# Performance work log

Hardware: AMD Instinct MI355X
Metric: run time of the kernel (lower is better)

Reference implementation:

```python
import jax, jax.numpy as jnp
import numpy as np

CUTOFF = 3.0   # self.cutoff
RMIN = 3.5     # rmin in cutoff_function (note rmin > cutoff, faithful to source)
ETA = 4.0
N_RADIAL = 5
N_3BODY = 12
NATOMS = 2048
K = 48         # neighbors per atom (equal counts -> ragged loop becomes dense batch)
HID = 64
NPAIRS = NATOMS * K


def setup_inputs() -> dict:
    key = jax.random.key(0)
    ks = jax.random.split(key, 4)
    # displacements scaled so |rij| is mostly within a few Angstrom
    rij = jax.random.normal(ks[0], (NPAIRS, 3), jnp.float32) * 1.5
    # sorted-by-atom pair list with K neighbors per atom
    unique_i = jnp.repeat(jnp.arange(NATOMS, dtype=jnp.int64), K)
    W1 = jax.random.normal(ks[1], (N_RADIAL + N_3BODY, HID), jnp.float32) * 0.1
    b1 = jnp.zeros((HID,), jnp.float32)
    W2 = jax.random.normal(ks[2], (HID, HID), jnp.float32) * 0.1
    b2 = jnp.zeros((HID,), jnp.float32)
    W3 = jax.random.normal(ks[3], (HID, 1), jnp.float32) * 0.1
    b3 = jnp.zeros((1,), jnp.float32)
    return dict(rij=rij, unique_i=unique_i, W1=W1, b1=b1, W2=W2, b2=b2, W3=W3, b3=b3)


def _energy(rij, W1, b1, W2, b2, W3, b3):
    d = jnp.linalg.norm(rij, axis=1, keepdims=True)           # (P,1)
    diff_norm = rij / jnp.maximum(d, 1e-12)                   # F.normalize
    # pair cutoff (rmin=3.5, c=3.0 as in source)
    fc = jnp.where(d > RMIN,
                   0.5 + 0.5 * jnp.cos(jnp.pi * (d - RMIN) / (CUTOFF - RMIN)),
                   1.0)
    # radial Bessel basis, n = 1..5
    ns = jnp.arange(1, N_RADIAL + 1, dtype=rij.dtype)
    rbf = jnp.sqrt(2.0 / CUTOFF) * jnp.sin(ns * jnp.pi / CUTOFF * d) / d * fc  # (P,5)
    # 3-body Gaussian descriptors
    fcrik = (0.5 + 0.5 * jnp.cos(jnp.pi * d / CUTOFF))[:, 0]  # (P,)
    dn = diff_norm.reshape(NATOMS, K, 3)
    cosang = jnp.einsum('nkd,nld->nkl', dn, dn)               # (N,K,K) pairwise mm
    cosang = jnp.where(jnp.eye(K, dtype=bool)[None], 0.0, cosang)  # fill_diagonal_(0)
    mu = jnp.linspace(-1.0, 1.0, N_3BODY).astype(rij.dtype)
    w = fcrik.reshape(NATOMS, 1, K, 1)                        # fcrik broadcast on axis being summed
    g3b = jnp.sum(jnp.exp(-ETA * (cosang[..., None] - mu) ** 2) * w, axis=2)  # (N,K,12)
    g3b = g3b.reshape(NPAIRS, N_3BODY)
    desc = jnp.concatenate([rbf, g3b], axis=1)                # (P,17)
    h = jnp.tanh(desc @ W1 + b1)
    h = jnp.tanh(h @ W2 + b2)
    eij = h @ W3 + b3                                         # (P,1)
    return jnp.sum(eij * fc)


def reference(rij, unique_i, W1, b1, W2, b2, W3, b3):
    # Module output: gradients of total energy w.r.t. rij (written into beta)
    return jax.grad(_energy)(rij, W1, b1, W2, b2, W3, b3)
```

## Files before the change

### kernel.cpp

```cpp
#include <hip/hip_runtime.h>
#include <hip/hip_bf16.h>

#define NATOMS 2048
#define K 48
#define NR 5
#define NM 12
#define ND 17
#define HID 64

#define PI_F 3.14159265358979f
#define CUT 3.0f
#define RMIN_F 3.5f
#define AFC (-6.28318530717959f)
#define POC (PI_F / CUT)
#define SQ 0.816496580927726f
#define CMC (-0.132231404958678f)
#define N4L (-5.77078016355585f)
#define E1L (2.09846551402031f)
#define TL2 (2.88539008177793f)

__device__ unsigned short g_w1t[64 * 32];
__device__ unsigned short g_w2t[64 * 64];
__device__ unsigned short g_w2r[64 * 64];
__device__ unsigned short g_w1r[32 * 64];

using frag_ab = __attribute__((ext_vector_type(8))) short;
using frag_cd = __attribute__((ext_vector_type(4))) float;
using f2 = __attribute__((ext_vector_type(2))) float;
using f4 = __attribute__((ext_vector_type(4))) float;

__device__ __forceinline__ float fast_tanh(float x) {
    const float t = __builtin_amdgcn_exp2f(TL2 * x);
    return 1.0f - 2.0f * __builtin_amdgcn_rcpf(t + 1.0f);
}

__device__ __forceinline__ unsigned short f2bs(float x) {
    __hip_bfloat16 b = __float2bfloat16(x);
    return __builtin_bit_cast(unsigned short, b);
}

__device__ __forceinline__ float bs2f(unsigned short u) {
    return __builtin_bit_cast(float, ((unsigned)u) << 16);
}

template <int CTRL>
__device__ __forceinline__ float dpp_add(float x) {
    const int y = __builtin_amdgcn_update_dpp(
        0, __builtin_bit_cast(int, x), CTRL, 0xF, 0xF, true);
    return x + __builtin_bit_cast(float, y);
}

__global__ __launch_bounds__(256) void k_prep(const float* __restrict__ W1,
                                              const float* __restrict__ W2) {
    const int i = blockIdx.x * 256 + threadIdx.x;
    if (i < 2048) {
        const int n = i >> 5, k = i & 31;
        g_w1t[i] = (k < ND) ? f2bs(W1[k * HID + n]) : (unsigned short)0;
    } else if (i < 2048 + 4096) {
        const int j = i - 2048, n = j >> 6, k = j & 63;
        g_w2t[j] = f2bs(W2[k * HID + n]);
    } else if (i < 2048 + 8192) {
        const int j = i - (2048 + 4096);
        g_w2r[j] = f2bs(W2[j]);
    } else if (i < 2048 + 8192 + 2048) {
        const int j = i - (2048 + 8192), n = j >> 6;
        g_w1r[j] = (n < ND) ? f2bs(W1[j]) : (unsigned short)0;
    }
}

#define H1_OFF   0
#define ST_OFF   0
#define DESC_OFF 6912
#define GZ2_OFF  6912
#define SGD_OFF  6912
#define SGF_OFF  10560
#define SGU_OFF  11328
#define SS_OFF   13824
#define SE_OFF   18528
#define SU_OFF   19296
#define SFC_OFF  20064
#define SFK_OFF  20256
#define SM_BYTES 20448

__global__ __launch_bounds__(256, 6) void k_fused(const float* __restrict__ rij,
                                                  const float* __restrict__ b1,
                                                  const float* __restrict__ b2,
                                                  const float* __restrict__ W3,
                                                  const float* __restrict__ b3,
                                                  float* __restrict__ out) {
    __shared__ __align__(16) char smem[SM_BYTES];
    short*          h1S   = (short*)(smem + H1_OFF);
    unsigned short* sT    = (unsigned short*)(smem + ST_OFF);
    short*          descS = (short*)(smem + DESC_OFF);
    short*          gz2S  = (short*)(smem + GZ2_OFF);
    float*          sgd   = (float*)(smem + SGD_OFF);
    float*          sgf4  = (float*)(smem + SGF_OFF);
    float*          sgu4  = (float*)(smem + SGU_OFF);
    unsigned short* sS    = (unsigned short*)(smem + SS_OFF);
    float*          se    = (float*)(smem + SE_OFF);
    float*          su    = (float*)(smem + SU_OFF);
    float*          sfc   = (float*)(smem + SFC_OFF);
    float*          sfk   = (float*)(smem + SFK_OFF);

    const int t = threadIdx.x;
    const int base3 = blockIdx.x * (K * 3);
    const int w = t >> 6, lane = t & 63, quad = lane >> 4, lm = lane & 15;
    const int n0 = w * 16 + lm;

    const frag_ab wf1  = *(const frag_ab*)&g_w1t[n0 * 32 + quad * 8];
    const frag_ab wf2a = *(const frag_ab*)&g_w2t[n0 * 64 + quad * 8];
    const frag_ab wf2b = *(const frag_ab*)&g_w2t[n0 * 64 + 32 + quad * 8];
    const frag_ab wr2a = *(const frag_ab*)&g_w2r[n0 * 64 + quad * 8];
    const frag_ab wr2b = *(const frag_ab*)&g_w2r[n0 * 64 + 32 + quad * 8];
    const float bias1 = b1[n0];
    const float bias2 = b2[n0];
    const float w3n   = W3[n0];
    const float b3v   = b3[0];

    if (t < K) {
        const float x = rij[base3 + 3 * t];
        const float y = rij[base3 + 3 * t + 1];
        const float z = rij[base3 + 3 * t + 2];
        float s2 = fmaxf(x * x + y * y + z * z, 1e-24f);
        const float inv = __builtin_amdgcn_rsqf(s2);
        const float d = s2 * inv;
        *(f4*)&su[4 * t] = (f4){x * inv, y * inv, z * inv, d};
        sfk[t] = 0.5f + 0.5f * __cosf(POC * d);
        const float fc = (d > RMIN_F) ? (0.5f + 0.5f * __cosf(AFC * (d - RMIN_F))) : 1.0f;
        sfc[t] = fc;
        float s1, c1;
        __sincosf(POC * d, &s1, &c1);
        const float sc = SQ * fc * inv;
        float sn = s1, cn = c1;
#pragma unroll 1
        for (int n = 0; n < NR; n++) {
            descS[t * 40 + n] = (short)f2bs(sc * sn);
            const float snx = sn * c1 + cn * s1;
            cn = cn * c1 - sn * s1;
            sn = snx;
        }
#pragma unroll 1
        for (int c = ND; c < 32; c++) descS[t * 40 + c] = 0;
    }
    __syncthreads();

    if (t < 192) {
        const int k = t >> 2, ch = t & 3;
        const f4 uk = *(const f4*)&su[4 * k];
        const float* sul = &su[4 * (ch * 12)];
        f2 partv[6];
#pragma unroll
        for (int i = 0; i < 6; i++) partv[i] = (f2){0.0f, 0.0f};
#pragma unroll 1
        for (int li = 0; li < 12; li++) {
            const int l = ch * 12 + li;
            const f4 ul = *(const f4*)&sul[4 * li];
            float c = uk.x * ul.x + uk.y * ul.y + uk.z * ul.z;
            if (k == l) c = 0.0f;
            const float cp1 = c + 1.0f;
            const float e0 = __builtin_amdgcn_exp2f(N4L * cp1 * cp1) * sfk[l];
            const float e1 = __builtin_amdgcn_exp2f(E1L * cp1);
            const float e2s = e1 * e1;
            const f2 e2v = {e2s, e2s};
            f2 tm = {e0, e0 * e1};
            partv[0] += tm;
#pragma unroll
            for (int i = 1; i < 6; i++) { tm *= e2v; partv[i] += tm; }
        }
#pragma unroll
        for (int i = 0; i < 6; i++) {
            partv[i].x = dpp_add<0x4E>(dpp_add<0xB1>(partv[i].x));
            partv[i].y = dpp_add<0x4E>(dpp_add<0xB1>(partv[i].y));
        }
        if (ch == 0) {
#pragma unroll
            for (int i = 0; i < 6; i++) {
                const int m0 = 2 * i, m1 = 2 * i + 1;
                descS[k * 40 + NR + m0] =
                    (short)f2bs(partv[i].x * __expf(CMC * (float)(m0 * m0)));
                descS[k * 40 + NR + m1] =
                    (short)f2bs(partv[i].y * __expf(CMC * (float)(m1 * m1)));
            }
        }
    }
    __syncthreads();

#pragma unroll 1
    for (int mt = 0; mt < 3; mt++) {
        const frag_ab a = *(const frag_ab*)&descS[(mt * 16 + lm) * 40 + quad * 8];
        frag_cd acc = {bias1, bias1, bias1, bias1};
        acc = __builtin_amdgcn_mfma_f32_16x16x32_bf16(a, wf1, acc, 0, 0, 0);
#pragma unroll
        for (int r = 0; r < 4; r++)
            h1S[(mt * 16 + quad * 4 + r) * 72 + n0] = (short)f2bs(fast_tanh(acc[r]));
    }
    __syncthreads();

#pragma unroll 1
    for (int mt = 0; mt < 3; mt++) {
        const frag_ab a0 = *(const frag_ab*)&h1S[(mt * 16 + lm) * 72 + quad * 8];
        const frag_ab a1 = *(const frag_ab*)&h1S[(mt * 16 + lm) * 72 + 32 + quad * 8];
        frag_cd acc = {bias2, bias2, bias2, bias2};
        acc = __builtin_amdgcn_mfma_f32_16x16x32_bf16(a0, wf2a, acc, 0, 0, 0);
        acc = __builtin_amdgcn_mfma_f32_16x16x32_bf16(a1, wf2b, acc, 0, 0, 0);
        float ep[4];
#pragma unroll
        for (int r = 0; r < 4; r++) {
            const int row = mt * 16 + quad * 4 + r;
            const float tv = fast_tanh(acc[r]);
            ep[r] = tv * w3n;
            gz2S[row * 72 + n0] = (short)f2bs(sfc[row] * w3n * (1.0f - tv * tv));
        }
#pragma unroll
        for (int r = 0; r < 4; r++)
            ep[r] = dpp_add<0x118>(dpp_add<0x114>(dpp_add<0x112>(dpp_add<0x111>(ep[r]))));
        if (lm == 15) {
#pragma unroll
            for (int r = 0; r < 4; r++) se[w * 48 + mt * 16 + quad * 4 + r] = ep[r];
        }
    }
    __syncthreads();

#pragma unroll 1
    for (int mt = 0; mt < 3; mt++) {
        const frag_ab a0 = *(const frag_ab*)&gz2S[(mt * 16 + lm) * 72 + quad * 8];
        const frag_ab a1 = *(const frag_ab*)&gz2S[(mt * 16 + lm) * 72 + 32 + quad * 8];
        frag_cd acc = {0.0f, 0.0f, 0.0f, 0.0f};
        acc = __builtin_amdgcn_mfma_f32_16x16x32_bf16(a0, wr2a, acc, 0, 0, 0);
        acc = __builtin_amdgcn_mfma_f32_16x16x32_bf16(a1, wr2b, acc, 0, 0, 0);
#pragma unroll
        for (int r = 0; r < 4; r++) {
            const int row = mt * 16 + quad * 4 + r;
            const float tv = bs2f((unsigned short)h1S[row * 72 + n0]);
            h1S[row * 72 + n0] = (short)f2bs(acc[r] * (1.0f - tv * tv));
        }
    }
    __syncthreads();

#pragma unroll 1
    for (int tid = w; tid < 6; tid += 4) {
        const int mt = tid >> 1, nt = tid & 1, n = nt * 16 + lm;
        const frag_ab b0 = *(const frag_ab*)&g_w1r[n * 64 + quad * 8];
        const frag_ab b1f = *(const frag_ab*)&g_w1r[n * 64 + 32 + quad * 8];
        const frag_ab a0 = *(const frag_ab*)&h1S[(mt * 16 + lm) * 72 + quad * 8];
        const frag_ab a1 = *(const frag_ab*)&h1S[(mt * 16 + lm) * 72 + 32 + quad * 8];
        frag_cd acc = {0.0f, 0.0f, 0.0f, 0.0f};
        acc = __builtin_amdgcn_mfma_f32_16x16x32_bf16(a0, b0, acc, 0, 0, 0);
        acc = __builtin_amdgcn_mfma_f32_16x16x32_bf16(a1, b1f, acc, 0, 0, 0);
        if (n < ND) {
            const int mm = n - NR;
            const float cmul = (n >= NR) ? __expf(CMC * (float)(mm * mm)) : 1.0f;
#pragma unroll
            for (int r = 0; r < 4; r++)
                sgd[(mt * 16 + quad * 4 + r) * 19 + n] = acc[r] * cmul;
        }
    }
    if (t < K)
        sgd[t * 19 + 17] = se[t] + se[48 + t] + se[96 + t] + se[144 + t] + b3v;
    __syncthreads();

    if (t < 192) {
        const int k = t >> 2, ch = t & 3;
        f2 gm[NM];
#pragma unroll
        for (int m = 0; m < NM; m++) {
            const float g = sgd[k * 19 + NR + m];
            gm[m] = (f2){g, (float)m * g};
        }
        const f4 uk = *(const f4*)&su[4 * k];
        const float* sul = &su[4 * (ch * 12)];
#pragma unroll 1
        for (int li = 0; li < 12; li++) {
            const int l = ch * 12 + li;
            const f4 ul = *(const f4*)&sul[4 * li];
            float c = uk.x * ul.x + uk.y * ul.y + uk.z * ul.z;
            if (k == l) c = 0.0f;
            const float cp1 = c + 1.0f;
            const float e0 = __builtin_amdgcn_exp2f(N4L * cp1 * cp1);
            const float x = __builtin_amdgcn_exp2f(E1L * cp1);
            const f2 xx = {x, x};
            f2 pd = gm[11];
#pragma unroll
            for (int m = 10; m >= 1; m--) pd = __builtin_elementwise_fma(pd, xx, gm[m]);
            const float Pv = fmaf(pd.x, x, gm[0].x);
            const float T = e0 * Pv;
            const float U = e0 * x * pd.y;
            const float Sp = fmaf(cp1, T, -(2.0f / 11.0f) * U);
            const float Sv = (k == l) ? 0.0f : (-8.0f) * Sp;
            sT[k * 49 + l] = f2bs(T);
            sS[k * 49 + l] = f2bs(Sv);
        }
    }
    __syncthreads();

    if (lane < K) {
        float s = 0.0f;
#pragma unroll 1
        for (int kk = 12 * w; kk < 12 * w + 12; kk++) s += bs2f(sT[kk * 49 + lane]);
        sgf4[w * 48 + lane] = s;

        const int k = lane;
        const float fk = sfk[k];
        float gx = 0.0f, gy = 0.0f, gz = 0.0f;
#pragma unroll 1
        for (int l = 12 * w; l < 12 * w + 12; l++) {
            const float wgt = fmaf(bs2f(sS[k * 49 + l]), sfk[l],
                                   bs2f(sS[l * 49 + k]) * fk);
            const f4 ul = *(const f4*)&su[4 * l];
            gx = fmaf(wgt, ul.x, gx);
            gy = fmaf(wgt, ul.y, gy);
            gz = fmaf(wgt, ul.z, gz);
        }
        sgu4[(w * 48 + k) * 3 + 0] = gx;
        sgu4[(w * 48 + k) * 3 + 1] = gy;
        sgu4[(w * 48 + k) * 3 + 2] = gz;
    }
    __syncthreads();

    if (t < K) {
        const float sgf_t = sgf4[t] + sgf4[48 + t] + sgf4[96 + t] + sgf4[144 + t];
        float gux = 0.0f, guy = 0.0f, guz = 0.0f;
#pragma unroll
        for (int ww = 0; ww < 4; ww++) {
            gux += sgu4[(ww * 48 + t) * 3 + 0];
            guy += sgu4[(ww * 48 + t) * 3 + 1];
            guz += sgu4[(ww * 48 + t) * 3 + 2];
        }
        const f4 uv = *(const f4*)&su[4 * t];
        const float d = uv.w;
        const float ux = uv.x, uy = uv.y, uz = uv.z;
        const float invd = __builtin_amdgcn_rcpf(d);
        float gfc = sgd[t * 19 + 17];
        float gdR = 0.0f;
        float s1, c1;
        __sincosf(POC * d, &s1, &c1);
        float sn = s1, cn = c1, bn = POC;
#pragma unroll 1
        for (int n = 0; n < NR; n++) {
            const float g = sgd[t * 19 + n];
            gfc = fmaf(g, SQ * sn * invd, gfc);
            gdR = fmaf(g, SQ * (bn * cn - sn * invd) * invd, gdR);
            const float snx = sn * c1 + cn * s1;
            cn = cn * c1 - sn * s1;
            sn = snx;
            bn += POC;
        }
        const float fc = sfc[t];
        float dfc = 0.0f;
        if (d > RMIN_F) dfc = -0.5f * AFC * __sinf(AFC * (d - RMIN_F));
        const float dfcrik = -0.5f * POC * __sinf(POC * d);

        const float gd = fc * gdR + gfc * dfc + sgf_t * dfcrik;
        const float dot = gux * ux + guy * uy + guz * uz;

        out[base3 + 3 * t + 0] = fmaf(gd, ux, (gux - dot * ux) * invd);
        out[base3 + 3 * t + 1] = fmaf(gd, uy, (guy - dot * uy) * invd);
        out[base3 + 3 * t + 2] = fmaf(gd, uz, (guz - dot * uz) * invd);
    }
}

extern "C" void kernel_launch(void* const* d_in, const int* in_sizes, int n_in,
                              void* d_out, int out_size, void* d_ws, size_t ws_size,
                              hipStream_t stream) {
    (void)in_sizes; (void)n_in; (void)out_size; (void)d_ws; (void)ws_size;
    const float* rij = (const float*)d_in[0];
    const float* W1 = (const float*)d_in[2];
    const float* b1 = (const float*)d_in[3];
    const float* W2 = (const float*)d_in[4];
    const float* b2 = (const float*)d_in[5];
    const float* W3 = (const float*)d_in[6];
    const float* b3 = (const float*)d_in[7];
    float* out = (float*)d_out;

    k_prep<<<48, 256, 0, stream>>>(W1, W2);
    k_fused<<<NATOMS, 256, 0, stream>>>(rij, b1, b2, W3, b3, out);
}
```

Baseline: 93.49 us.

## Run each atom's block as a single wavefront without barriers

Shrinks each atom's block from four wavefronts to one 64-lane wavefront that does all MLP column tiles itself, which removes every __syncthreads and the cross-wave partial-sum buffers. The 3-body forward and backward loops now walk all 48 neighbors per lane instead of splitting across four lanes. Intermediate T/S matrices are stored transposed, so the symmetric gradient term is built from one direct accumulation plus a vectorized row read. The cost is less parallelism per atom, longer serial loops per lane and higher register pressure, traded against more resident blocks per CU.

```diff
diff --git a/kernel.cpp b/kernel.cpp
--- a/kernel.cpp
+++ b/kernel.cpp
@@ -28,6 +28,7 @@
 using frag_cd = __attribute__((ext_vector_type(4))) float;
 using f2 = __attribute__((ext_vector_type(2))) float;
 using f4 = __attribute__((ext_vector_type(4))) float;
+using s4 = __attribute__((ext_vector_type(4))) short;
 
 __device__ __forceinline__ float fast_tanh(float x) {
     const float t = __builtin_amdgcn_exp2f(TL2 * x);
@@ -69,92 +70,81 @@
 }
 
 #define H1_OFF   0
-#define ST_OFF   0
-#define DESC_OFF 6912
+#define TT_OFF   0
+#define SST_OFF  4992
 #define GZ2_OFF  6912
-#define SGD_OFF  6912
-#define SGF_OFF  10560
-#define SGU_OFF  11328
-#define SS_OFF   13824
-#define SE_OFF   18528
-#define SU_OFF   19296
-#define SFC_OFF  20064
-#define SFK_OFF  20256
-#define SM_BYTES 20448
-
-__global__ __launch_bounds__(256, 6) void k_fused(const float* __restrict__ rij,
-                                                  const float* __restrict__ b1,
-                                                  const float* __restrict__ b2,
-                                                  const float* __restrict__ W3,
-                                                  const float* __restrict__ b3,
-                                                  float* __restrict__ out) {
+#define DESC_OFF 13824
+#define SGD_OFF  13824
+#define SU_OFF   17664
+#define SFC_OFF  18432
+#define SFK_OFF  18624
+#define SM_BYTES 18816
+
+__global__ __launch_bounds__(64, 2) void k_fused(const float* __restrict__ rij,
+                                                 const float* __restrict__ b1,
+                                                 const float* __restrict__ b2,
+                                                 const float* __restrict__ W3,
+                                                 const float* __restrict__ b3,
+                                                 float* __restrict__ out) {
     __shared__ __align__(16) char smem[SM_BYTES];
     short*          h1S   = (short*)(smem + H1_OFF);
-    unsigned short* sT    = (unsigned short*)(smem + ST_OFF);
+    unsigned short* tT    = (unsigned short*)(smem + TT_OFF);
+    unsigned short* tS    = (unsigned short*)(smem + SST_OFF);
+    short*          gz2S  = (short*)(smem + GZ2_OFF);
     short*          descS = (short*)(smem + DESC_OFF);
-    short*          gz2S  = (short*)(smem + GZ2_OFF);
     float*          sgd   = (float*)(smem + SGD_OFF);
-    float*          sgf4  = (float*)(smem + SGF_OFF);
-    float*          sgu4  = (float*)(smem + SGU_OFF);
-    unsigned short* sS    = (unsigned short*)(smem + SS_OFF);
-    float*          se    = (float*)(smem + SE_OFF);
     float*          su    = (float*)(smem + SU_OFF);
     float*          sfc   = (float*)(smem + SFC_OFF);
     float*          sfk   = (float*)(smem + SFK_OFF);
 
-    const int t = threadIdx.x;
+    const int lane = threadIdx.x;
+    const int quad = lane >> 4, lm = lane & 15;
     const int base3 = blockIdx.x * (K * 3);
-    const int w = t >> 6, lane = t & 63, quad = lane >> 4, lm = lane & 15;
-    const int n0 = w * 16 + lm;
-
-    const frag_ab wf1  = *(const frag_ab*)&g_w1t[n0 * 32 + quad * 8];
-    const frag_ab wf2a = *(const frag_ab*)&g_w2t[n0 * 64 + quad * 8];
-    const frag_ab wf2b = *(const frag_ab*)&g_w2t[n0 * 64 + 32 + quad * 8];
-    const frag_ab wr2a = *(const frag_ab*)&g_w2r[n0 * 64 + quad * 8];
-    const frag_ab wr2b = *(const frag_ab*)&g_w2r[n0 * 64 + 32 + quad * 8];
-    const float bias1 = b1[n0];
-    const float bias2 = b2[n0];
-    const float w3n   = W3[n0];
-    const float b3v   = b3[0];
-
-    if (t < K) {
-        const float x = rij[base3 + 3 * t];
-        const float y = rij[base3 + 3 * t + 1];
-        const float z = rij[base3 + 3 * t + 2];
+
+    float b1v[4], b2v[4], w3v[4];
+#pragma unroll
+    for (int nt = 0; nt < 4; nt++) {
+        b1v[nt] = b1[nt * 16 + lm];
+        b2v[nt] = b2[nt * 16 + lm];
+        w3v[nt] = W3[nt * 16 + lm];
+    }
+    const float b3v = b3[0];
+
+    if (lane < K) {
+        const float x = rij[base3 + 3 * lane];
+        const float y = rij[base3 + 3 * lane + 1];
+        const float z = rij[base3 + 3 * lane + 2];
         float s2 = fmaxf(x * x + y * y + z * z, 1e-24f);
         const float inv = __builtin_amdgcn_rsqf(s2);
         const float d = s2 * inv;
-        *(f4*)&su[4 * t] = (f4){x * inv, y * inv, z * inv, d};
-        sfk[t] = 0.5f + 0.5f * __cosf(POC * d);
+        *(f4*)&su[4 * lane] = (f4){x * inv, y * inv, z * inv, d};
+        sfk[lane] = 0.5f + 0.5f * __cosf(POC * d);
         const float fc = (d > RMIN_F) ? (0.5f + 0.5f * __cosf(AFC * (d - RMIN_F))) : 1.0f;
-        sfc[t] = fc;
+        sfc[lane] = fc;
         float s1, c1;
         __sincosf(POC * d, &s1, &c1);
         const float sc = SQ * fc * inv;
         float sn = s1, cn = c1;
 #pragma unroll 1
         for (int n = 0; n < NR; n++) {
-            descS[t * 40 + n] = (short)f2bs(sc * sn);
+            descS[lane * 40 + n] = (short)f2bs(sc * sn);
             const float snx = sn * c1 + cn * s1;
             cn = cn * c1 - sn * s1;
             sn = snx;
         }
 #pragma unroll 1
-        for (int c = ND; c < 32; c++) descS[t * 40 + c] = 0;
-    }
-    __syncthreads();
-
-    if (t < 192) {
-        const int k = t >> 2, ch = t & 3;
+        for (int c = ND; c < 32; c++) descS[lane * 40 + c] = 0;
+    }
+
+    if (lane < K) {
+        const int k = lane;
         const f4 uk = *(const f4*)&su[4 * k];
-        const float* sul = &su[4 * (ch * 12)];
         f2 partv[6];
 #pragma unroll
         for (int i = 0; i < 6; i++) partv[i] = (f2){0.0f, 0.0f};
 #pragma unroll 1
-        for (int li = 0; li < 12; li++) {
-            const int l = ch * 12 + li;
-            const f4 ul = *(const f4*)&sul[4 * li];
+        for (int l = 0; l < K; l++) {
+            const f4 ul = *(const f4*)&su[4 * l];
             float c = uk.x * ul.x + uk.y * ul.y + uk.z * ul.z;
             if (k == l) c = 0.0f;
             const float cp1 = c + 1.0f;
@@ -169,110 +159,144 @@
         }
 #pragma unroll
         for (int i = 0; i < 6; i++) {
-            partv[i].x = dpp_add<0x4E>(dpp_add<0xB1>(partv[i].x));
-            partv[i].y = dpp_add<0x4E>(dpp_add<0xB1>(partv[i].y));
-        }
-        if (ch == 0) {
-#pragma unroll
-            for (int i = 0; i < 6; i++) {
-                const int m0 = 2 * i, m1 = 2 * i + 1;
-                descS[k * 40 + NR + m0] =
-                    (short)f2bs(partv[i].x * __expf(CMC * (float)(m0 * m0)));
-                descS[k * 40 + NR + m1] =
-                    (short)f2bs(partv[i].y * __expf(CMC * (float)(m1 * m1)));
-            }
-        }
-    }
-    __syncthreads();
-
-#pragma unroll 1
-    for (int mt = 0; mt < 3; mt++) {
-        const frag_ab a = *(const frag_ab*)&descS[(mt * 16 + lm) * 40 + quad * 8];
-        frag_cd acc = {bias1, bias1, bias1, bias1};
-        acc = __builtin_amdgcn_mfma_f32_16x16x32_bf16(a, wf1, acc, 0, 0, 0);
-#pragma unroll
-        for (int r = 0; r < 4; r++)
-            h1S[(mt * 16 + quad * 4 + r) * 72 + n0] = (short)f2bs(fast_tanh(acc[r]));
-    }
-    __syncthreads();
-
-#pragma unroll 1
-    for (int mt = 0; mt < 3; mt++) {
-        const frag_ab a0 = *(const frag_ab*)&h1S[(mt * 16 + lm) * 72 + quad * 8];
-        const frag_ab a1 = *(const frag_ab*)&h1S[(mt * 16 + lm) * 72 + 32 + quad * 8];
-        frag_cd acc = {bias2, bias2, bias2, bias2};
-        acc = __builtin_amdgcn_mfma_f32_16x16x32_bf16(a0, wf2a, acc, 0, 0, 0);
-        acc = __builtin_amdgcn_mfma_f32_16x16x32_bf16(a1, wf2b, acc, 0, 0, 0);
-        float ep[4];
-#pragma unroll
-        for (int r = 0; r < 4; r++) {
-            const int row = mt * 16 + quad * 4 + r;
-            const float tv = fast_tanh(acc[r]);
-            ep[r] = tv * w3n;
-            gz2S[row * 72 + n0] = (short)f2bs(sfc[row] * w3n * (1.0f - tv * tv));
-        }
-#pragma unroll
-        for (int r = 0; r < 4; r++)
-            ep[r] = dpp_add<0x118>(dpp_add<0x114>(dpp_add<0x112>(dpp_add<0x111>(ep[r]))));
-        if (lm == 15) {
-#pragma unroll
-            for (int r = 0; r < 4; r++) se[w * 48 + mt * 16 + quad * 4 + r] = ep[r];
-        }
-    }
-    __syncthreads();
-
-#pragma unroll 1
-    for (int mt = 0; mt < 3; mt++) {
-        const frag_ab a0 = *(const frag_ab*)&gz2S[(mt * 16 + lm) * 72 + quad * 8];
-        const frag_ab a1 = *(const frag_ab*)&gz2S[(mt * 16 + lm) * 72 + 32 + quad * 8];
-        frag_cd acc = {0.0f, 0.0f, 0.0f, 0.0f};
-        acc = __builtin_amdgcn_mfma_f32_16x16x32_bf16(a0, wr2a, acc, 0, 0, 0);
-        acc = __builtin_amdgcn_mfma_f32_16x16x32_bf16(a1, wr2b, acc, 0, 0, 0);
-#pragma unroll
-        for (int r = 0; r < 4; r++) {
-            const int row = mt * 16 + quad * 4 + r;
-            const float tv = bs2f((unsigned short)h1S[row * 72 + n0]);
-            h1S[row * 72 + n0] = (short)f2bs(acc[r] * (1.0f - tv * tv));
-        }
-    }
-    __syncthreads();
-
-#pragma unroll 1
-    for (int tid = w; tid < 6; tid += 4) {
-        const int mt = tid >> 1, nt = tid & 1, n = nt * 16 + lm;
-        const frag_ab b0 = *(const frag_ab*)&g_w1r[n * 64 + quad * 8];
-        const frag_ab b1f = *(const frag_ab*)&g_w1r[n * 64 + 32 + quad * 8];
-        const frag_ab a0 = *(const frag_ab*)&h1S[(mt * 16 + lm) * 72 + quad * 8];
-        const frag_ab a1 = *(const frag_ab*)&h1S[(mt * 16 + lm) * 72 + 32 + quad * 8];
-        frag_cd acc = {0.0f, 0.0f, 0.0f, 0.0f};
-        acc = __builtin_amdgcn_mfma_f32_16x16x32_bf16(a0, b0, acc, 0, 0, 0);
-        acc = __builtin_amdgcn_mfma_f32_16x16x32_bf16(a1, b1f, acc, 0, 0, 0);
-        if (n < ND) {
-            const int mm = n - NR;
-            const float cmul = (n >= NR) ? __expf(CMC * (float)(mm * mm)) : 1.0f;
+            const int m0 = 2 * i, m1 = 2 * i + 1;
+            descS[k * 40 + NR + m0] = (short)f2bs(partv[i].x * __expf(CMC * (float)(m0 * m0)));
+            descS[k * 40 + NR + m1] = (short)f2bs(partv[i].y * __expf(CMC * (float)(m1 * m1)));
+        }
+    }
+
+    {
+        frag_ab wf1[4];
+#pragma unroll
+        for (int nt = 0; nt < 4; nt++)
+            wf1[nt] = *(const frag_ab*)&g_w1t[(nt * 16 + lm) * 32 + quad * 8];
+#pragma unroll 1
+        for (int mt = 0; mt < 3; mt++) {
+            const frag_ab a = *(const frag_ab*)&descS[(mt * 16 + lm) * 40 + quad * 8];
+#pragma unroll
+            for (int nt = 0; nt < 4; nt++) {
+                frag_cd acc = {b1v[nt], b1v[nt], b1v[nt], b1v[nt]};
+                acc = __builtin_amdgcn_mfma_f32_16x16x32_bf16(a, wf1[nt], acc, 0, 0, 0);
+#pragma unroll
+                for (int r = 0; r < 4; r++)
+                    h1S[(mt * 16 + quad * 4 + r) * 72 + nt * 16 + lm] =
+                        (short)f2bs(fast_tanh(acc[r]));
+            }
+        }
+    }
+
+    {
+        frag_ab wa[4], wb[4];
+#pragma unroll
+        for (int nt = 0; nt < 4; nt++) {
+            wa[nt] = *(const frag_ab*)&g_w2t[(nt * 16 + lm) * 64 + quad * 8];
+            wb[nt] = *(const frag_ab*)&g_w2t[(nt * 16 + lm) * 64 + 32 + quad * 8];
+        }
+#pragma unroll 1
+        for (int mt = 0; mt < 3; mt++) {
+            const frag_ab a0 = *(const frag_ab*)&h1S[(mt * 16 + lm) * 72 + quad * 8];
+            const frag_ab a1 = *(const frag_ab*)&h1S[(mt * 16 + lm) * 72 + 32 + quad * 8];
+            const f4 fcv = *(const f4*)&sfc[mt * 16 + quad * 4];
+            float ep[4] = {0.0f, 0.0f, 0.0f, 0.0f};
+#pragma unroll
+            for (int nt = 0; nt < 4; nt++) {
+                frag_cd acc = {b2v[nt], b2v[nt], b2v[nt], b2v[nt]};
+                acc = __builtin_amdgcn_mfma_f32_16x16x32_bf16(a0, wa[nt], acc, 0, 0, 0);
+                acc = __builtin_amdgcn_mfma_f32_16x16x32_bf16(a1, wb[nt], acc, 0, 0, 0);
+#pragma unroll
+                for (int r = 0; r < 4; r++) {
+                    const int row = mt * 16 + quad * 4 + r;
+                    const float tv = fast_tanh(acc[r]);
+                    ep[r] = fmaf(tv, w3v[nt], ep[r]);
+                    gz2S[row * 72 + nt * 16 + lm] =
+                        (short)f2bs(fcv[r] * w3v[nt] * (1.0f - tv * tv));
+                }
+            }
 #pragma unroll
             for (int r = 0; r < 4; r++)
-                sgd[(mt * 16 + quad * 4 + r) * 19 + n] = acc[r] * cmul;
-        }
-    }
-    if (t < K)
-        sgd[t * 19 + 17] = se[t] + se[48 + t] + se[96 + t] + se[144 + t] + b3v;
-    __syncthreads();
-
-    if (t < 192) {
-        const int k = t >> 2, ch = t & 3;
+                ep[r] = dpp_add<0x118>(dpp_add<0x114>(dpp_add<0x112>(dpp_add<0x111>(ep[r]))));
+            if (lm == 15) {
+#pragma unroll
+                for (int r = 0; r < 4; r++)
+                    sgd[(mt * 16 + quad * 4 + r) * 20 + 17] = ep[r] + b3v;
+            }
+        }
+    }
+
+    {
+        frag_ab wa[4], wb[4];
+#pragma unroll
+        for (int nt = 0; nt < 4; nt++) {
+            wa[nt] = *(const frag_ab*)&g_w2r[(nt * 16 + lm) * 64 + quad * 8];
+            wb[nt] = *(const frag_ab*)&g_w2r[(nt * 16 + lm) * 64 + 32 + quad * 8];
+        }
+#pragma unroll 1
+        for (int mt = 0; mt < 3; mt++) {
+            const frag_ab a0 = *(const frag_ab*)&gz2S[(mt * 16 + lm) * 72 + quad * 8];
+            const frag_ab a1 = *(const frag_ab*)&gz2S[(mt * 16 + lm) * 72 + 32 + quad * 8];
+#pragma unroll
+            for (int nt = 0; nt < 4; nt++) {
+                frag_cd acc = {0.0f, 0.0f, 0.0f, 0.0f};
+                acc = __builtin_amdgcn_mfma_f32_16x16x32_bf16(a0, wa[nt], acc, 0, 0, 0);
+                acc = __builtin_amdgcn_mfma_f32_16x16x32_bf16(a1, wb[nt], acc, 0, 0, 0);
+#pragma unroll
+                for (int r = 0; r < 4; r++) {
+                    const int idx = (mt * 16 + quad * 4 + r) * 72 + nt * 16 + lm;
+                    const float tv = bs2f((unsigned short)h1S[idx]);
+                    h1S[idx] = (short)f2bs(acc[r] * (1.0f - tv * tv));
+                }
+            }
+        }
+    }
+
+    {
+        frag_ab wa[2], wb[2];
+#pragma unroll
+        for (int nt = 0; nt < 2; nt++) {
+            wa[nt] = *(const frag_ab*)&g_w1r[(nt * 16 + lm) * 64 + quad * 8];
+            wb[nt] = *(const frag_ab*)&g_w1r[(nt * 16 + lm) * 64 + 32 + quad * 8];
+        }
+        const float cm0 = (lm >= NR)
+            ? __expf(CMC * (float)((lm - NR) * (lm - NR))) : 1.0f;
+        const float cm1 = __expf(-16.0f);
+#pragma unroll 1
+        for (int mt = 0; mt < 3; mt++) {
+            const frag_ab a0 = *(const frag_ab*)&h1S[(mt * 16 + lm) * 72 + quad * 8];
+            const frag_ab a1 = *(const frag_ab*)&h1S[(mt * 16 + lm) * 72 + 32 + quad * 8];
+            {
+                frag_cd acc = {0.0f, 0.0f, 0.0f, 0.0f};
+                acc = __builtin_amdgcn_mfma_f32_16x16x32_bf16(a0, wa[0], acc, 0, 0, 0);
+                acc = __builtin_amdgcn_mfma_f32_16x16x32_bf16(a1, wb[0], acc, 0, 0, 0);
+#pragma unroll
+                for (int r = 0; r < 4; r++)
+                    sgd[(mt * 16 + quad * 4 + r) * 20 + lm] = acc[r] * cm0;
+            }
+            {
+                frag_cd acc = {0.0f, 0.0f, 0.0f, 0.0f};
+                acc = __builtin_amdgcn_mfma_f32_16x16x32_bf16(a0, wa[1], acc, 0, 0, 0);
+                acc = __builtin_amdgcn_mfma_f32_16x16x32_bf16(a1, wb[1], acc, 0, 0, 0);
+                if (lm == 0) {
+#pragma unroll
+                    for (int r = 0; r < 4; r++)
+                        sgd[(mt * 16 + quad * 4 + r) * 20 + 16] = acc[r] * cm1;
+                }
+            }
+        }
+    }
+
+    float gx1 = 0.0f, gy1 = 0.0f, gz1 = 0.0f;
+    if (lane < K) {
+        const int k = lane;
         f2 gm[NM];
 #pragma unroll
         for (int m = 0; m < NM; m++) {
-            const float g = sgd[k * 19 + NR + m];
+            const float g = sgd[k * 20 + NR + m];
             gm[m] = (f2){g, (float)m * g};
         }
         const f4 uk = *(const f4*)&su[4 * k];
-        const float* sul = &su[4 * (ch * 12)];
-#pragma unroll 1
-        for (int li = 0; li < 12; li++) {
-            const int l = ch * 12 + li;
-            const f4 ul = *(const f4*)&sul[4 * li];
+#pragma unroll 1
+        for (int l = 0; l < K; l++) {
+            const f4 ul = *(const f4*)&su[4 * l];
             float c = uk.x * ul.x + uk.y * ul.y + uk.z * ul.z;
             if (k == l) c = 0.0f;
             const float cp1 = c + 1.0f;
@@ -287,57 +311,50 @@
             const float U = e0 * x * pd.y;
             const float Sp = fmaf(cp1, T, -(2.0f / 11.0f) * U);
             const float Sv = (k == l) ? 0.0f : (-8.0f) * Sp;
-            sT[k * 49 + l] = f2bs(T);
-            sS[k * 49 + l] = f2bs(Sv);
-        }
-    }
-    __syncthreads();
+            tT[l * 52 + k] = f2bs(T);
+            tS[l * 52 + k] = f2bs(Sv);
+            const float A = Sv * sfk[l];
+            gx1 = fmaf(A, ul.x, gx1);
+            gy1 = fmaf(A, ul.y, gy1);
+            gz1 = fmaf(A, ul.z, gz1);
+        }
+    }
 
     if (lane < K) {
-        float s = 0.0f;
-#pragma unroll 1
-        for (int kk = 12 * w; kk < 12 * w + 12; kk++) s += bs2f(sT[kk * 49 + lane]);
-        sgf4[w * 48 + lane] = s;
-
         const int k = lane;
+        float sgf_t = 0.0f, gx2 = 0.0f, gy2 = 0.0f, gz2v = 0.0f;
+#pragma unroll 1
+        for (int i = 0; i < 12; i++) {
+            const s4 tv4 = *(const s4*)&tT[k * 52 + 4 * i];
+            const s4 sv4 = *(const s4*)&tS[k * 52 + 4 * i];
+#pragma unroll
+            for (int j = 0; j < 4; j++) {
+                const int l = 4 * i + j;
+                const f4 ul = *(const f4*)&su[4 * l];
+                sgf_t += bs2f((unsigned short)tv4[j]);
+                const float Sv = bs2f((unsigned short)sv4[j]);
+                gx2 = fmaf(Sv, ul.x, gx2);
+                gy2 = fmaf(Sv, ul.y, gy2);
+                gz2v = fmaf(Sv, ul.z, gz2v);
+            }
+        }
         const float fk = sfk[k];
-        float gx = 0.0f, gy = 0.0f, gz = 0.0f;
-#pragma unroll 1
-        for (int l = 12 * w; l < 12 * w + 12; l++) {
-            const float wgt = fmaf(bs2f(sS[k * 49 + l]), sfk[l],
-                                   bs2f(sS[l * 49 + k]) * fk);
-            const f4 ul = *(const f4*)&su[4 * l];
-            gx = fmaf(wgt, ul.x, gx);
-            gy = fmaf(wgt, ul.y, gy);
-            gz = fmaf(wgt, ul.z, gz);
-        }
-        sgu4[(w * 48 + k) * 3 + 0] = gx;
-        sgu4[(w * 48 + k) * 3 + 1] = gy;
-        sgu4[(w * 48 + k) * 3 + 2] = gz;
-    }
-    __syncthreads();
-
-    if (t < K) {
-        const float sgf_t = sgf4[t] + sgf4[48 + t] + sgf4[96 + t] + sgf4[144 + t];
-        float gux = 0.0f, guy = 0.0f, guz = 0.0f;
-#pragma unroll
-        for (int ww = 0; ww < 4; ww++) {
-            gux += sgu4[(ww * 48 + t) * 3 + 0];
-            guy += sgu4[(ww * 48 + t) * 3 + 1];
-            guz += sgu4[(ww * 48 + t) * 3 + 2];
-        }
-        const f4 uv = *(const f4*)&su[4 * t];
+        const float gux = gx1 + fk * gx2;
+        const float guy = gy1 + fk * gy2;
+        const float guz = gz1 + fk * gz2v;
+
+        const f4 uv = *(const f4*)&su[4 * k];
         const float d = uv.w;
         const float ux = uv.x, uy = uv.y, uz = uv.z;
         const float invd = __builtin_amdgcn_rcpf(d);
-        float gfc = sgd[t * 19 + 17];
+        float gfc = sgd[k * 20 + 17];
         float gdR = 0.0f;
         float s1, c1;
         __sincosf(POC * d, &s1, &c1);
         float sn = s1, cn = c1, bn = POC;
 #pragma unroll 1
         for (int n = 0; n < NR; n++) {
-            const float g = sgd[t * 19 + n];
+            const float g = sgd[k * 20 + n];
             gfc = fmaf(g, SQ * sn * invd, gfc);
             gdR = fmaf(g, SQ * (bn * cn - sn * invd) * invd, gdR);
             const float snx = sn * c1 + cn * s1;
@@ -345,7 +362,7 @@
             sn = snx;
             bn += POC;
         }
-        const float fc = sfc[t];
+        const float fc = sfc[k];
         float dfc = 0.0f;
         if (d > RMIN_F) dfc = -0.5f * AFC * __sinf(AFC * (d - RMIN_F));
         const float dfcrik = -0.5f * POC * __sinf(POC * d);
@@ -353,9 +370,9 @@
         const float gd = fc * gdR + gfc * dfc + sgf_t * dfcrik;
         const float dot = gux * ux + guy * uy + guz * uz;
 
-        out[base3 + 3 * t + 0] = fmaf(gd, ux, (gux - dot * ux) * invd);
-        out[base3 + 3 * t + 1] = fmaf(gd, uy, (guy - dot * uy) * invd);
-        out[base3 + 3 * t + 2] = fmaf(gd, uz, (guz - dot * uz) * invd);
+        out[base3 + 3 * k + 0] = fmaf(gd, ux, (gux - dot * ux) * invd);
+        out[base3 + 3 * k + 1] = fmaf(gd, uy, (guy - dot * uy) * invd);
+        out[base3 + 3 * k + 2] = fmaf(gd, uz, (guz - dot * uz) * invd);
     }
 }
 
@@ -373,5 +390,5 @@
     float* out = (float*)d_out;
 
     k_prep<<<48, 256, 0, stream>>>(W1, W2);
-    k_fused<<<NATOMS, 256, 0, stream>>>(rij, b1, b2, W3, b3, out);
-}
+    k_fused<<<NATOMS, 64, 0, stream>>>(rij, b1, b2, W3, b3, out);
+}
```

Result: no change. 94.57 us (+1.1%).
